# Optimization experiments

Hardware: AMD Instinct MI355X
Metric: run time of the kernel (lower is better)

Reference implementation:

```python
import jax, jax.numpy as jnp
import numpy as np

DIM = 256
B = 8
H = 56
W = 56
K = 2
EPS = 1e-5  # torch BatchNorm2d default eps


def _conv1x1(x, w, b):
    # x: [B,C,H,W], w: [O,C], b: [O]
    return jnp.einsum('oc,bchw->bohw', w, x) + b[None, :, None, None]


def _bn(x, g, be, m, v):
    # inference-mode BatchNorm2d with running stats
    s = g / jnp.sqrt(v + EPS)
    return x * s[None, :, None, None] + (be - m * s)[None, :, None, None]


def _grapher(x, w1, b1, g1, be1, m1, v1, wg, bg, gg, beg, mg, vg, w2, b2, g2, be2, m2, v2):
    # fc1: 1x1 conv + BN
    h = _bn(_conv1x1(x, w1, b1), g1, be1, m1, v1)
    Hh, Ww = h.shape[2], h.shape[3]
    # MRConv4d: running max over circular-shift differences
    # torch.cat([x[:,:,-i:,:], x[:,:,:-i,:]], dim=2) == jnp.roll(x, i, axis=2)
    xj = jnp.zeros_like(h)

    def body_h(c, i):
        return jnp.maximum(c, h - jnp.roll(h, i, axis=2)), None

    xj, _ = jax.lax.scan(body_h, xj, jnp.arange(K, Hh, K))

    def body_w(c, i):
        return jnp.maximum(c, h - jnp.roll(h, i, axis=3)), None

    xj, _ = jax.lax.scan(body_w, xj, jnp.arange(K, Ww, K))

    cat = jnp.concatenate([h, xj], axis=1)  # [B, 2*dim, H, W]
    # MRConv4d.nn: Conv2d(2*dim, 2*dim, 1) -> BN(2*dim) -> GELU (exact erf)
    g = jax.nn.gelu(_bn(_conv1x1(cat, wg, bg), gg, beg, mg, vg), approximate=False)
    # fc2: Conv2d(2*dim, dim, 1) + BN(dim), then residual
    return _bn(_conv1x1(g, w2, b2), g2, be2, m2, v2) + x


def setup_inputs() -> dict:
    key = jax.random.key(0)
    ks = jax.random.split(key, 12)
    d, d2 = DIM, 2 * DIM

    def w(k, o, c):
        return jax.random.normal(k, (o, c), jnp.float32) * np.float32(1.0 / np.sqrt(c))

    return {
        'x': jax.random.normal(ks[0], (B, d, H, W), jnp.float32),
        'w1': w(ks[1], d, d), 'b1': jnp.zeros((d,), jnp.float32),
        'g1': jnp.ones((d,), jnp.float32), 'be1': jnp.zeros((d,), jnp.float32),
        'm1': jax.random.normal(ks[2], (d,), jnp.float32) * 0.1,
        'v1': jax.random.uniform(ks[3], (d,), jnp.float32, 0.5, 1.5),
        'wg': w(ks[4], d2, d2), 'bg': jnp.zeros((d2,), jnp.float32),
        'gg': jnp.ones((d2,), jnp.float32), 'beg': jnp.zeros((d2,), jnp.float32),
        'mg': jax.random.normal(ks[5], (d2,), jnp.float32) * 0.1,
        'vg': jax.random.uniform(ks[6], (d2,), jnp.float32, 0.5, 1.5),
        'w2': w(ks[7], d, d2), 'b2': jnp.zeros((d,), jnp.float32),
        'g2': jnp.ones((d,), jnp.float32), 'be2': jnp.zeros((d,), jnp.float32),
        'm2': jax.random.normal(ks[8], (d,), jnp.float32) * 0.1,
        'v2': jax.random.uniform(ks[9], (d,), jnp.float32, 0.5, 1.5),
    }


def reference(x, w1, b1, g1, be1, m1, v1, wg, bg, gg, beg, mg, vg, w2, b2, g2, be2, m2, v2):
    return _grapher(x, w1, b1, g1, be1, m1, v1, wg, bg, gg, beg, mg, vg, w2, b2, g2, be2, m2, v2)
```

## Files before the change

### kernel.cpp

```cpp
#include <hip/hip_runtime.h>
#include <math.h>

#define SPB 3136
#define NB 8
#define MTOT (NB*SPB)
#define EPS 1e-5f

typedef unsigned short u16;
typedef __attribute__((ext_vector_type(8))) short short8;
typedef __attribute__((ext_vector_type(4))) float float4v;

__device__ __forceinline__ float b2f(u16 v){ unsigned u=((unsigned)v)<<16; float f; __builtin_memcpy(&f,&u,4); return f; }
__device__ __forceinline__ u16 f2b(float f){ unsigned u; __builtin_memcpy(&u,&f,4); u += 0x7fffu + ((u>>16)&1u); return (u16)(u>>16); }
__device__ __forceinline__ float gelu_f(float z){
  float t = 1.5957691216f * z * (1.0f + 0.044715f*z*z);
  return __fdividef(z, 1.0f + __expf(-t));
}

__device__ __forceinline__ void gll16(const u16* g, u16* l){
  __builtin_amdgcn_global_load_lds((const __attribute__((address_space(1))) void*)g,
                                   (__attribute__((address_space(3))) void*)l, 16, 0, 0);
}

__global__ void prep_consts_k(const float* b1,const float* g1,const float* be1,const float* m1,const float* v1,
                              const float* bg,const float* gg,const float* beg,const float* mg,const float* vg,
                              const float* b2,const float* g2,const float* be2,const float* m2,const float* v2,
                              float* cst){
  int i = threadIdx.x;
  if (i < 256) {
    float s = g1[i]*rsqrtf(v1[i]+EPS);
    cst[i] = s; cst[256+i] = b1[i]*s + be1[i] - m1[i]*s;
    float s2 = g2[i]*rsqrtf(v2[i]+EPS);
    cst[1536+i] = s2; cst[1792+i] = b2[i]*s2 + be2[i] - m2[i]*s2;
  }
  float s = gg[i]*rsqrtf(vg[i]+EPS);
  cst[512+i] = s; cst[1024+i] = bg[i]*s + beg[i] - mg[i]*s;
}

__global__ void conv_w_k(const float* __restrict__ w1,const float* __restrict__ wg,const float* __restrict__ w2,
                         u16* __restrict__ w1b,u16* __restrict__ wgb,u16* __restrict__ w2b){
  int i = blockIdx.x*256 + threadIdx.x;
  if (i < 65536)  w1b[i] = f2b(w1[i]);
  if (i < 262144) wgb[i] = f2b(wg[i]);
  if (i < 131072) w2b[i] = f2b(w2[i]);
}

__global__ void transpose_x_k(const float* __restrict__ x, u16* __restrict__ xt){
  __shared__ float t[32][33];
  int b = blockIdx.z, ct = blockIdx.y, st = blockIdx.x;
  int ts = threadIdx.x, tc = threadIdx.y;
  #pragma unroll
  for (int i=0;i<4;i++){
    int c = tc + i*8;
    t[c][ts] = x[((size_t)(b*256 + ct*32 + c))*SPB + st*32 + ts];
  }
  __syncthreads();
  #pragma unroll
  for (int i=0;i<4;i++){
    int r = tc + i*8;
    xt[((size_t)(b*SPB + st*32 + r))*256 + ct*32 + ts] = f2b(t[ts][r]);
  }
}

__global__ void rowmin_k(const u16* __restrict__ cat, float* __restrict__ rmin){
  int b = blockIdx.x/56, y = blockIdx.x%56, c = threadIdx.x;
  float mE=3.4e38f, mO=3.4e38f;
  const u16* base = cat + ((size_t)(b*SPB + y*56))*512 + c;
  for (int x=0;x<56;x+=2){
    mE = fminf(mE, b2f(base[(size_t)x*512]));
    mO = fminf(mO, b2f(base[(size_t)(x+1)*512]));
  }
  rmin[((size_t)(b*2+0)*56 + y)*256 + c]=mE;
  rmin[((size_t)(b*2+1)*56 + y)*256 + c]=mO;
}
__global__ void colmin_k(const u16* __restrict__ cat, float* __restrict__ cmin){
  int b = blockIdx.x/56, x = blockIdx.x%56, c = threadIdx.x;
  float mE=3.4e38f, mO=3.4e38f;
  const u16* base = cat + ((size_t)(b*SPB + x))*512 + c;
  for (int y=0;y<56;y+=2){
    mE = fminf(mE, b2f(base[(size_t)(y*56)*512]));
    mO = fminf(mO, b2f(base[(size_t)((y+1)*56)*512]));
  }
  cmin[((size_t)(b*2+0)*56 + x)*256 + c]=mE;
  cmin[((size_t)(b*2+1)*56 + x)*256 + c]=mO;
}
__global__ __launch_bounds__(256) void xj_k(u16* __restrict__ cat, const float* __restrict__ rmin, const float* __restrict__ cmin){
  int b = blockIdx.y;
  int t = threadIdx.x;
  int s = blockIdx.x*8 + (t>>5);
  int c0 = (t&31)*8;
  int y = s/56, x = s%56;
  size_t idx = ((size_t)(b*SPB + s))*512;
  short8 h8 = *(const short8*)&cat[idx + c0];
  const float* cp = &cmin[((size_t)(b*2+(y&1))*56 + x)*256 + c0];
  const float* rp = &rmin[((size_t)(b*2+(x&1))*56 + y)*256 + c0];
  float4v cv0 = *(const float4v*)cp, cv1 = *(const float4v*)(cp+4);
  float4v rv0 = *(const float4v*)rp, rv1 = *(const float4v*)(rp+4);
  short8 o;
  #pragma unroll
  for (int j=0;j<8;j++){
    float cm = (j<4) ? cv0[j] : cv1[j-4];
    float rm = (j<4) ? rv0[j] : rv1[j-4];
    o[j] = (short)f2b(fmaxf(0.0f, b2f((u16)h8[j]) - fminf(cm, rm)));
  }
  *(short8*)&cat[idx + 256 + c0] = o;
}

template<int KTOT, int EPI>
__global__ __launch_bounds__(256) void gemm_k(
    const u16* __restrict__ Ain, const u16* __restrict__ Wt,
    const float* __restrict__ scale, const float* __restrict__ bias,
    void* __restrict__ outp, const float* __restrict__ resid)
{
  __shared__ __align__(16) u16 smem[24576];
  const int tid = threadIdx.x;
  const int m0 = blockIdx.x * 128;
  const int o0 = blockIdx.y * 128;
  const int lane = tid & 63, wid = tid >> 6;
  const int quad = lane >> 4, l16 = lane & 15;
  const int wm = wid & 1, wn = wid >> 1;

  float4v acc[4][4];
  #pragma unroll
  for (int i=0;i<4;i++)
    #pragma unroll
    for (int j=0;j<4;j++) acc[i][j] = (float4v){0.f,0.f,0.f,0.f};

  const int row = tid >> 2, q8 = (tid & 3) * 8;
  const u16* ga0 = Ain + ((size_t)(m0 + row))*KTOT + q8;
  const u16* ga1 = ga0 + (size_t)64*KTOT;
  const u16* gb0 = Wt  + ((size_t)(o0 + row))*KTOT + q8;
  const u16* gb1 = gb0 + (size_t)64*KTOT;
  u16* l8 = smem + tid*8;

  auto STAGE = [&](int kt, int buf){
    u16* b_ = l8 + buf*8192;
    gll16(ga0 + kt, b_);
    gll16(ga1 + kt, b_ + 2048);
    gll16(gb0 + kt, b_ + 4096);
    gll16(gb1 + kt, b_ + 6144);
  };
  auto COMPUTE = [&](int buf){
    const u16* A_ = smem + buf*8192;
    const u16* B_ = A_ + 4096;
    short8 af[4], bfr[4];
    #pragma unroll
    for (int im=0;im<4;im++) af[im]  = *(const short8*)&A_[(wm*64+im*16+l16)*32 + quad*8];
    #pragma unroll
    for (int in=0;in<4;in++) bfr[in] = *(const short8*)&B_[(wn*64+in*16+l16)*32 + quad*8];
    #pragma unroll
    for (int im=0;im<4;im++)
      #pragma unroll
      for (int in=0;in<4;in++)
        acc[im][in] = __builtin_amdgcn_mfma_f32_16x16x32_bf16(af[im], bfr[in], acc[im][in], 0, 0, 0);
  };

  constexpr int NIT = KTOT / 32;
  STAGE(0, 0);
  STAGE(32, 1);
  #pragma unroll
  for (int t = 0; t < NIT; ++t) {
    __builtin_amdgcn_sched_barrier(0);
    if (t + 1 < NIT) asm volatile("s_waitcnt vmcnt(4) lgkmcnt(0)" ::: "memory");
    else             asm volatile("s_waitcnt vmcnt(0) lgkmcnt(0)" ::: "memory");
    __builtin_amdgcn_s_barrier();
    __builtin_amdgcn_sched_barrier(0);
    if (t + 2 < NIT) STAGE((t+2)*32, (t+2)%3);
    COMPUTE(t%3);
  }
  __syncthreads();

  if (EPI == 1 || EPI == 2) {
    u16* tile = smem;
    #pragma unroll
    for (int im=0;im<4;im++)
      #pragma unroll
      for (int in=0;in<4;in++){
        int ol = wn*64 + in*16 + l16;
        float sc = scale[o0+ol], bi = bias[o0+ol];
        #pragma unroll
        for (int r=0;r<4;r++){
          float v = acc[im][in][r]*sc + bi;
          if (EPI==2) v = gelu_f(v);
          tile[(wm*64+im*16+quad*4+r)*128 + ol] = f2b(v);
        }
      }
    __syncthreads();
    u16* op = (u16*)outp;
    #pragma unroll
    for (int p=0;p<8;p++){
      int chunk = p*256 + tid;
      int rr = chunk >> 4, off = (chunk & 15)*8;
      *(uint4*)&op[((size_t)(m0 + rr))*512 + o0 + off] = *(const uint4*)&tile[rr*128 + off];
    }
  } else {
    float* ftile = (float*)smem;
    float* op = (float*)outp;
    #pragma unroll
    for (int h=0; h<2; h++){
      if (wn == h){
        #pragma unroll
        for (int im=0;im<4;im++)
          #pragma unroll
          for (int in=0;in<4;in++){
            int c64 = in*16 + l16;
            int og = o0 + h*64 + c64;
            float sc = scale[og], bi = bias[og];
            float4v v;
            #pragma unroll
            for (int r=0;r<4;r++) v[r] = acc[im][in][r]*sc + bi;
            *(float4v*)&ftile[c64*132 + wm*64 + im*16 + quad*4] = v;
          }
      }
      __syncthreads();
      #pragma unroll
      for (int p=0;p<8;p++){
        int chunk = p*256 + tid;
        int rr = chunk >> 5, off = (chunk & 31)*4;
        int m = m0 + off;
        int b = m / SPB, s = m - b*SPB;
        size_t g = ((size_t)(b*256 + o0 + h*64 + rr))*SPB + s;
        float4v v = *(const float4v*)&ftile[rr*132 + off];
        v.x += resid[g]; v.y += resid[g+1]; v.z += resid[g+2]; v.w += resid[g+3];
        *(float4v*)&op[g] = v;
      }
      __syncthreads();
    }
  }
}

extern "C" void kernel_launch(void* const* d_in, const int* in_sizes, int n_in,
                              void* d_out, int out_size, void* d_ws, size_t ws_size,
                              hipStream_t stream)
{
  const float* x  = (const float*)d_in[0];
  const float* w1 = (const float*)d_in[1];
  const float* b1 = (const float*)d_in[2];
  const float* g1 = (const float*)d_in[3];
  const float* be1= (const float*)d_in[4];
  const float* m1 = (const float*)d_in[5];
  const float* v1 = (const float*)d_in[6];
  const float* wg = (const float*)d_in[7];
  const float* bg = (const float*)d_in[8];
  const float* gg = (const float*)d_in[9];
  const float* beg= (const float*)d_in[10];
  const float* mg = (const float*)d_in[11];
  const float* vg = (const float*)d_in[12];
  const float* w2 = (const float*)d_in[13];
  const float* b2 = (const float*)d_in[14];
  const float* g2 = (const float*)d_in[15];
  const float* be2= (const float*)d_in[16];
  const float* m2 = (const float*)d_in[17];
  const float* v2 = (const float*)d_in[18];

  char* ws = (char*)d_ws;
  size_t off = 0;
  auto alloc = [&](size_t bytes){ void* p = ws + off; off += (bytes + 255) & ~(size_t)255; return p; };
  u16* xt    = (u16*)alloc((size_t)MTOT*256*2);
  u16* catt  = (u16*)alloc((size_t)MTOT*512*2);
  u16* gt    = (u16*)alloc((size_t)MTOT*512*2);
  u16* w1b   = (u16*)alloc((size_t)65536*2);
  u16* wgb   = (u16*)alloc((size_t)262144*2);
  u16* w2b   = (u16*)alloc((size_t)131072*2);
  float* cst = (float*)alloc((size_t)2048*4);
  float* rmin= (float*)alloc((size_t)NB*2*56*256*4);
  float* cmin= (float*)alloc((size_t)NB*2*56*256*4);

  hipLaunchKernelGGL(prep_consts_k, dim3(1), dim3(512), 0, stream,
                     b1,g1,be1,m1,v1, bg,gg,beg,mg,vg, b2,g2,be2,m2,v2, cst);
  hipLaunchKernelGGL(conv_w_k, dim3(1024), dim3(256), 0, stream, w1,wg,w2, w1b,wgb,w2b);
  hipLaunchKernelGGL(transpose_x_k, dim3(98,8,8), dim3(32,8), 0, stream, x, xt);
  hipLaunchKernelGGL((gemm_k<256,1>), dim3(196,2), dim3(256), 0, stream,
                     xt, w1b, cst+0, cst+256, (void*)catt, (const float*)nullptr);
  hipLaunchKernelGGL(rowmin_k, dim3(NB*56), dim3(256), 0, stream, catt, rmin);
  hipLaunchKernelGGL(colmin_k, dim3(NB*56), dim3(256), 0, stream, catt, cmin);
  hipLaunchKernelGGL(xj_k, dim3(392, NB), dim3(256), 0, stream, catt, rmin, cmin);
  hipLaunchKernelGGL((gemm_k<512,2>), dim3(196,4), dim3(256), 0, stream,
                     catt, wgb, cst+512, cst+1024, (void*)gt, (const float*)nullptr);
  hipLaunchKernelGGL((gemm_k<512,3>), dim3(196,2), dim3(256), 0, stream,
                     gt, w2b, cst+1536, cst+1792, d_out, x);
}
```

Baseline: 186.6 us.

## Enlarge GEMM tiles to 256x128 with LDS swizzle and merge small kernels

The GEMM block tile grows from 128x128 to 256x128. Each wave now owns a 64x128 slab, with 32 accumulators per thread, and launch bounds are set to 2 blocks per CU. The LDS layout is XOR-swizzled on the k-quad index to cut bank conflicts on fragment reads. The row-min and column-min kernels are merged into one launch, and constant prep is merged with weight conversion, to drop launches. The larger tile raises register and LDS pressure and halves the number of blocks (98 per column of tiles instead of 196), which may hurt occupancy and load balance across 256 CUs.

```diff
diff --git a/kernel.cpp b/kernel.cpp
--- a/kernel.cpp
+++ b/kernel.cpp
@@ -22,27 +22,25 @@
                                    (__attribute__((address_space(3))) void*)l, 16, 0, 0);
 }
 
-__global__ void prep_consts_k(const float* b1,const float* g1,const float* be1,const float* m1,const float* v1,
-                              const float* bg,const float* gg,const float* beg,const float* mg,const float* vg,
-                              const float* b2,const float* g2,const float* be2,const float* m2,const float* v2,
-                              float* cst){
-  int i = threadIdx.x;
+__global__ void prep_w_k(const float* __restrict__ w1,const float* __restrict__ wg,const float* __restrict__ w2,
+                         const float* b1,const float* g1,const float* be1,const float* m1,const float* v1,
+                         const float* bg,const float* gg,const float* beg,const float* mg,const float* vg,
+                         const float* b2,const float* g2,const float* be2,const float* m2,const float* v2,
+                         u16* __restrict__ w1b,u16* __restrict__ wgb,u16* __restrict__ w2b,float* cst){
+  int i = blockIdx.x*256 + threadIdx.x;
+  if (i < 65536)  w1b[i] = f2b(w1[i]);
+  if (i < 262144) wgb[i] = f2b(wg[i]);
+  if (i < 131072) w2b[i] = f2b(w2[i]);
   if (i < 256) {
     float s = g1[i]*rsqrtf(v1[i]+EPS);
     cst[i] = s; cst[256+i] = b1[i]*s + be1[i] - m1[i]*s;
     float s2 = g2[i]*rsqrtf(v2[i]+EPS);
     cst[1536+i] = s2; cst[1792+i] = b2[i]*s2 + be2[i] - m2[i]*s2;
   }
-  float s = gg[i]*rsqrtf(vg[i]+EPS);
-  cst[512+i] = s; cst[1024+i] = bg[i]*s + beg[i] - mg[i]*s;
-}
-
-__global__ void conv_w_k(const float* __restrict__ w1,const float* __restrict__ wg,const float* __restrict__ w2,
-                         u16* __restrict__ w1b,u16* __restrict__ wgb,u16* __restrict__ w2b){
-  int i = blockIdx.x*256 + threadIdx.x;
-  if (i < 65536)  w1b[i] = f2b(w1[i]);
-  if (i < 262144) wgb[i] = f2b(wg[i]);
-  if (i < 131072) w2b[i] = f2b(w2[i]);
+  if (i < 512) {
+    float s = gg[i]*rsqrtf(vg[i]+EPS);
+    cst[512+i] = s; cst[1024+i] = bg[i]*s + beg[i] - mg[i]*s;
+  }
 }
 
 __global__ void transpose_x_k(const float* __restrict__ x, u16* __restrict__ xt){
@@ -62,28 +60,25 @@
   }
 }
 
-__global__ void rowmin_k(const u16* __restrict__ cat, float* __restrict__ rmin){
-  int b = blockIdx.x/56, y = blockIdx.x%56, c = threadIdx.x;
-  float mE=3.4e38f, mO=3.4e38f;
-  const u16* base = cat + ((size_t)(b*SPB + y*56))*512 + c;
-  for (int x=0;x<56;x+=2){
-    mE = fminf(mE, b2f(base[(size_t)x*512]));
-    mO = fminf(mO, b2f(base[(size_t)(x+1)*512]));
-  }
-  rmin[((size_t)(b*2+0)*56 + y)*256 + c]=mE;
-  rmin[((size_t)(b*2+1)*56 + y)*256 + c]=mO;
-}
-__global__ void colmin_k(const u16* __restrict__ cat, float* __restrict__ cmin){
-  int b = blockIdx.x/56, x = blockIdx.x%56, c = threadIdx.x;
-  float mE=3.4e38f, mO=3.4e38f;
-  const u16* base = cat + ((size_t)(b*SPB + x))*512 + c;
-  for (int y=0;y<56;y+=2){
-    mE = fminf(mE, b2f(base[(size_t)(y*56)*512]));
-    mO = fminf(mO, b2f(base[(size_t)((y+1)*56)*512]));
-  }
-  cmin[((size_t)(b*2+0)*56 + x)*256 + c]=mE;
-  cmin[((size_t)(b*2+1)*56 + x)*256 + c]=mO;
-}
+__global__ void minmax_k(const u16* __restrict__ cat, float* __restrict__ rmin, float* __restrict__ cmin){
+  int b = blockIdx.x/56, i = blockIdx.x%56, c = threadIdx.x;
+  int col = blockIdx.y;
+  const u16* base; size_t stride;
+  if (!col){ base = cat + ((size_t)(b*SPB + i*56))*512 + c; stride = 512; }
+  else     { base = cat + ((size_t)(b*SPB + i))*512 + c;    stride = (size_t)56*512; }
+  float a0=3.4e38f,a1=3.4e38f,a2=3.4e38f,a3=3.4e38f;
+  for (int j=0;j<56;j+=4){
+    a0 = fminf(a0, b2f(base[(size_t)j*stride]));
+    a1 = fminf(a1, b2f(base[(size_t)(j+1)*stride]));
+    a2 = fminf(a2, b2f(base[(size_t)(j+2)*stride]));
+    a3 = fminf(a3, b2f(base[(size_t)(j+3)*stride]));
+  }
+  float mE = fminf(a0,a2), mO = fminf(a1,a3);
+  float* out = col ? cmin : rmin;
+  out[((size_t)(b*2+0)*56 + i)*256 + c]=mE;
+  out[((size_t)(b*2+1)*56 + i)*256 + c]=mO;
+}
+
 __global__ __launch_bounds__(256) void xj_k(u16* __restrict__ cat, const float* __restrict__ rmin, const float* __restrict__ cmin){
   int b = blockIdx.y;
   int t = threadIdx.x;
@@ -107,51 +102,53 @@
 }
 
 template<int KTOT, int EPI>
-__global__ __launch_bounds__(256) void gemm_k(
+__global__ __launch_bounds__(256,2) void gemm_k(
     const u16* __restrict__ Ain, const u16* __restrict__ Wt,
     const float* __restrict__ scale, const float* __restrict__ bias,
     void* __restrict__ outp, const float* __restrict__ resid)
 {
-  __shared__ __align__(16) u16 smem[24576];
+  __shared__ __align__(16) u16 smem[36864];
   const int tid = threadIdx.x;
-  const int m0 = blockIdx.x * 128;
+  const int m0 = blockIdx.x * 256;
   const int o0 = blockIdx.y * 128;
   const int lane = tid & 63, wid = tid >> 6;
   const int quad = lane >> 4, l16 = lane & 15;
-  const int wm = wid & 1, wn = wid >> 1;
-
-  float4v acc[4][4];
+
+  float4v acc[4][8];
   #pragma unroll
   for (int i=0;i<4;i++)
     #pragma unroll
-    for (int j=0;j<4;j++) acc[i][j] = (float4v){0.f,0.f,0.f,0.f};
-
-  const int row = tid >> 2, q8 = (tid & 3) * 8;
-  const u16* ga0 = Ain + ((size_t)(m0 + row))*KTOT + q8;
-  const u16* ga1 = ga0 + (size_t)64*KTOT;
-  const u16* gb0 = Wt  + ((size_t)(o0 + row))*KTOT + q8;
-  const u16* gb1 = gb0 + (size_t)64*KTOT;
+    for (int j=0;j<8;j++) acc[i][j] = (float4v){0.f,0.f,0.f,0.f};
+
+  const int row = tid >> 2;
+  const int q8s = ((tid & 3) ^ ((tid >> 3) & 3)) * 8;
+  const u16* ga0 = Ain + ((size_t)(m0 + row))*KTOT + q8s;
+  const u16* gb0 = Wt  + ((size_t)(o0 + row))*KTOT + q8s;
   u16* l8 = smem + tid*8;
 
   auto STAGE = [&](int kt, int buf){
-    u16* b_ = l8 + buf*8192;
-    gll16(ga0 + kt, b_);
-    gll16(ga1 + kt, b_ + 2048);
-    gll16(gb0 + kt, b_ + 4096);
-    gll16(gb1 + kt, b_ + 6144);
+    u16* b_ = l8 + buf*12288;
+    gll16(ga0 + kt,                     b_);
+    gll16(ga0 + (size_t) 64*KTOT + kt,  b_ + 2048);
+    gll16(ga0 + (size_t)128*KTOT + kt,  b_ + 4096);
+    gll16(ga0 + (size_t)192*KTOT + kt,  b_ + 6144);
+    gll16(gb0 + kt,                     b_ + 8192);
+    gll16(gb0 + (size_t) 64*KTOT + kt,  b_ + 10240);
   };
+  const int swz = (l16 >> 1) & 3;
   auto COMPUTE = [&](int buf){
-    const u16* A_ = smem + buf*8192;
-    const u16* B_ = A_ + 4096;
-    short8 af[4], bfr[4];
-    #pragma unroll
-    for (int im=0;im<4;im++) af[im]  = *(const short8*)&A_[(wm*64+im*16+l16)*32 + quad*8];
-    #pragma unroll
-    for (int in=0;in<4;in++) bfr[in] = *(const short8*)&B_[(wn*64+in*16+l16)*32 + quad*8];
+    const u16* A_ = smem + buf*12288;
+    const u16* B_ = A_ + 8192;
+    const int kq = (quad ^ swz) * 8;
+    short8 af[4], bfr[8];
+    #pragma unroll
+    for (int im=0;im<4;im++) af[im]  = *(const short8*)&A_[(wid*64+im*16+l16)*32 + kq];
+    #pragma unroll
+    for (int in=0;in<8;in++) bfr[in] = *(const short8*)&B_[(in*16+l16)*32 + kq];
     #pragma unroll
     for (int im=0;im<4;im++)
       #pragma unroll
-      for (int in=0;in<4;in++)
+      for (int in=0;in<8;in++)
         acc[im][in] = __builtin_amdgcn_mfma_f32_16x16x32_bf16(af[im], bfr[in], acc[im][in], 0, 0, 0);
   };
 
@@ -161,7 +158,7 @@
   #pragma unroll
   for (int t = 0; t < NIT; ++t) {
     __builtin_amdgcn_sched_barrier(0);
-    if (t + 1 < NIT) asm volatile("s_waitcnt vmcnt(4) lgkmcnt(0)" ::: "memory");
+    if (t + 1 < NIT) asm volatile("s_waitcnt vmcnt(6) lgkmcnt(0)" ::: "memory");
     else             asm volatile("s_waitcnt vmcnt(0) lgkmcnt(0)" ::: "memory");
     __builtin_amdgcn_s_barrier();
     __builtin_amdgcn_sched_barrier(0);
@@ -175,20 +172,20 @@
     #pragma unroll
     for (int im=0;im<4;im++)
       #pragma unroll
-      for (int in=0;in<4;in++){
-        int ol = wn*64 + in*16 + l16;
+      for (int in=0;in<8;in++){
+        int ol = in*16 + l16;
         float sc = scale[o0+ol], bi = bias[o0+ol];
         #pragma unroll
         for (int r=0;r<4;r++){
           float v = acc[im][in][r]*sc + bi;
           if (EPI==2) v = gelu_f(v);
-          tile[(wm*64+im*16+quad*4+r)*128 + ol] = f2b(v);
+          tile[(wid*64+im*16+quad*4+r)*128 + ol] = f2b(v);
         }
       }
     __syncthreads();
     u16* op = (u16*)outp;
     #pragma unroll
-    for (int p=0;p<8;p++){
+    for (int p=0;p<16;p++){
       int chunk = p*256 + tid;
       int rr = chunk >> 4, off = (chunk & 15)*8;
       *(uint4*)&op[((size_t)(m0 + rr))*512 + o0 + off] = *(const uint4*)&tile[rr*128 + off];
@@ -198,29 +195,28 @@
     float* op = (float*)outp;
     #pragma unroll
     for (int h=0; h<2; h++){
-      if (wn == h){
+      #pragma unroll
+      for (int im=0;im<4;im++)
         #pragma unroll
-        for (int im=0;im<4;im++)
+        for (int in4=0;in4<4;in4++){
+          int in = h*4 + in4;
+          int c64 = in4*16 + l16;
+          int og = o0 + h*64 + c64;
+          float sc = scale[og], bi = bias[og];
+          float4v v;
           #pragma unroll
-          for (int in=0;in<4;in++){
-            int c64 = in*16 + l16;
-            int og = o0 + h*64 + c64;
-            float sc = scale[og], bi = bias[og];
-            float4v v;
-            #pragma unroll
-            for (int r=0;r<4;r++) v[r] = acc[im][in][r]*sc + bi;
-            *(float4v*)&ftile[c64*132 + wm*64 + im*16 + quad*4] = v;
-          }
-      }
+          for (int r=0;r<4;r++) v[r] = acc[im][in][r]*sc + bi;
+          *(float4v*)&ftile[c64*260 + wid*64 + im*16 + quad*4] = v;
+        }
       __syncthreads();
       #pragma unroll
-      for (int p=0;p<8;p++){
+      for (int p=0;p<16;p++){
         int chunk = p*256 + tid;
-        int rr = chunk >> 5, off = (chunk & 31)*4;
+        int rr = chunk >> 6, off = (chunk & 63)*4;
         int m = m0 + off;
         int b = m / SPB, s = m - b*SPB;
         size_t g = ((size_t)(b*256 + o0 + h*64 + rr))*SPB + s;
-        float4v v = *(const float4v*)&ftile[rr*132 + off];
+        float4v v = *(const float4v*)&ftile[rr*260 + off];
         v.x += resid[g]; v.y += resid[g+1]; v.z += resid[g+2]; v.w += resid[g+3];
         *(float4v*)&op[g] = v;
       }
@@ -266,17 +262,16 @@
   float* rmin= (float*)alloc((size_t)NB*2*56*256*4);
   float* cmin= (float*)alloc((size_t)NB*2*56*256*4);
 
-  hipLaunchKernelGGL(prep_consts_k, dim3(1), dim3(512), 0, stream,
-                     b1,g1,be1,m1,v1, bg,gg,beg,mg,vg, b2,g2,be2,m2,v2, cst);
-  hipLaunchKernelGGL(conv_w_k, dim3(1024), dim3(256), 0, stream, w1,wg,w2, w1b,wgb,w2b);
+  hipLaunchKernelGGL(prep_w_k, dim3(1024), dim3(256), 0, stream,
+                     w1,wg,w2, b1,g1,be1,m1,v1, bg,gg,beg,mg,vg, b2,g2,be2,m2,v2,
+                     w1b,wgb,w2b, cst);
   hipLaunchKernelGGL(transpose_x_k, dim3(98,8,8), dim3(32,8), 0, stream, x, xt);
-  hipLaunchKernelGGL((gemm_k<256,1>), dim3(196,2), dim3(256), 0, stream,
+  hipLaunchKernelGGL((gemm_k<256,1>), dim3(98,2), dim3(256), 0, stream,
                      xt, w1b, cst+0, cst+256, (void*)catt, (const float*)nullptr);
-  hipLaunchKernelGGL(rowmin_k, dim3(NB*56), dim3(256), 0, stream, catt, rmin);
-  hipLaunchKernelGGL(colmin_k, dim3(NB*56), dim3(256), 0, stream, catt, cmin);
+  hipLaunchKernelGGL(minmax_k, dim3(NB*56,2), dim3(256), 0, stream, catt, rmin, cmin);
   hipLaunchKernelGGL(xj_k, dim3(392, NB), dim3(256), 0, stream, catt, rmin, cmin);
-  hipLaunchKernelGGL((gemm_k<512,2>), dim3(196,4), dim3(256), 0, stream,
+  hipLaunchKernelGGL((gemm_k<512,2>), dim3(98,4), dim3(256), 0, stream,
                      catt, wgb, cst+512, cst+1024, (void*)gt, (const float*)nullptr);
-  hipLaunchKernelGGL((gemm_k<512,3>), dim3(196,2), dim3(256), 0, stream,
+  hipLaunchKernelGGL((gemm_k<512,3>), dim3(98,2), dim3(256), 0, stream,
                      gt, w2b, cst+1536, cst+1792, d_out, x);
 }
```

Measured after the change: 189.5 us. About the same (+1.6%).
